# Kernel tuning notes

Measured on AMD Instinct MI355X. Metric: run time of the kernel, lower is better.

Reference implementation:

```python
import jax, jax.numpy as jnp
import numpy as np

N_EXPERTS = 8
D_MODEL = 1024
D_FF = 2048
NUM_TOKENS = 16384


def setup_inputs() -> dict:
    key = jax.random.key(0)
    k1, k2, k3, k4 = jax.random.split(key, 4)
    x = jax.random.normal(k1, (NUM_TOKENS, D_MODEL), dtype=jnp.float32)
    expert_indices = jax.random.randint(k2, (NUM_TOKENS,), 0, N_EXPERTS, dtype=jnp.int32)
    # init per nn.init.normal_(std=0.02)
    gate_up_weight = 0.02 * jax.random.normal(k3, (N_EXPERTS, 2 * D_FF, D_MODEL), dtype=jnp.float32)
    down_weight = 0.02 * jax.random.normal(k4, (N_EXPERTS, D_MODEL, D_FF), dtype=jnp.float32)
    return {"x": x, "expert_indices": expert_indices,
            "gate_up_weight": gate_up_weight, "down_weight": down_weight}


def reference(x, expert_indices, gate_up_weight, down_weight):
    # Faithful math: each token t uses expert e = expert_indices[t]:
    #   combined = x @ gate_up_weight[e].T ; gate, up = split ; h = silu(gate)*up
    #   out = h @ down_weight[e].T
    # Implemented as a fixed loop over the (small) expert set with masked
    # accumulation, avoiding the original's per-token [2F,D] weight gather.
    n_experts = gate_up_weight.shape[0]
    d_ff = down_weight.shape[2]
    out = jnp.zeros((x.shape[0], down_weight.shape[1]), dtype=x.dtype)
    for e in range(n_experts):
        combined = x @ gate_up_weight[e].T                  # [T, 2*d_ff]
        gate, up = combined[:, :d_ff], combined[:, d_ff:]
        hidden = jax.nn.silu(gate) * up                     # [T, d_ff]
        o = hidden @ down_weight[e].T                       # [T, d_model]
        out = out + jnp.where((expert_indices == e)[:, None], o, 0.0)
    return out
```

## Files before the change

### kernel.cpp

```cpp
#include <hip/hip_runtime.h>

#define NTOK 16384
#define DM 1024
#define DFF 2048
#define NE 8

typedef unsigned short u16;
typedef __attribute__((ext_vector_type(8))) short bf16x8;
typedef __attribute__((ext_vector_type(4))) float f32x4;

__device__ __forceinline__ u16 f2bf(float f) {
  unsigned u = __float_as_uint(f);
  u += 0x7fff + ((u >> 16) & 1);
  return (u16)(u >> 16);
}

__device__ __forceinline__ void async16(const void* g, void* l) {
  __builtin_amdgcn_global_load_lds(
      (const __attribute__((address_space(1))) unsigned int*)g,
      (__attribute__((address_space(3))) unsigned int*)l, 16, 0, 0);
}

__global__ void k_count(const int* __restrict__ idx, int* __restrict__ counts) {
  int t = blockIdx.x * 256 + threadIdx.x;
  atomicAdd(&counts[idx[t]], 1);
}

__global__ void k_offsets(int* __restrict__ c) {
  if (threadIdx.x == 0) {
    int acc = 0;
    for (int e = 0; e < NE; e++) { c[8 + e] = acc; c[16 + e] = acc; acc += c[e]; }
  }
}

__global__ void k_scatter(const int* __restrict__ idx, int* __restrict__ cursor,
                          int* __restrict__ tl) {
  int t = blockIdx.x * 256 + threadIdx.x;
  int pos = atomicAdd(&cursor[idx[t]], 1);
  tl[pos] = t;
}

__global__ void k_cvt_all(const float* __restrict__ x, const float* __restrict__ wgu,
                          const float* __restrict__ wd, u16* __restrict__ xb,
                          u16* __restrict__ wgub, u16* __restrict__ wdb) {
  const size_t N1 = (size_t)NTOK * DM;
  const size_t N2 = (size_t)NE * 2 * DFF * DM;
  const size_t N3 = (size_t)NE * DM * DFF;
  const size_t total4 = (N1 + N2 + N3) / 4;
  for (size_t q = (size_t)blockIdx.x * 256 + threadIdx.x; q < total4;
       q += (size_t)gridDim.x * 256) {
    size_t i = q * 4;
    const float* s;
    u16* d;
    if (i < N1) { s = x + i; d = xb + i; }
    else if (i < N1 + N2) { s = wgu + (i - N1); d = wgub + (i - N1); }
    else { s = wd + (i - N1 - N2); d = wdb + (i - N1 - N2); }
    float4 v = *(const float4*)s;
    ushort4 o;
    o.x = f2bf(v.x); o.y = f2bf(v.y); o.z = f2bf(v.z); o.w = f2bf(v.w);
    *(ushort4*)d = o;
  }
}

__global__ __launch_bounds__(512, 2) void k_gemm1(
    const u16* __restrict__ xb, const u16* __restrict__ wgu,
    u16* __restrict__ hid, const int* __restrict__ tl,
    const int* __restrict__ offs, const int* __restrict__ counts) {
  int wg = blockIdx.x;
  int e = wg & 7;
  int r = wg >> 3;
  int bx = r >> 4;
  int by = r & 15;
  int Me = counts[e];
  int m0 = bx * 256;
  if (m0 >= Me) return;
  int n0 = by * 128;
  int oe = offs[e];
  const int* tle = tl + oe;

  int tid = threadIdx.x;
  int lane = tid & 63;
  int wid = tid >> 6;
  int wm = wid >> 2;
  int wn = wid & 3;

  __shared__ u16 lds[2][2][256 * 64];

  int lr = lane >> 3;
  int swz = ((lane & 7) ^ lr) * 8;
  const u16* pA[4];
  const u16* pB[4];
#pragma unroll
  for (int j = 0; j < 4; j++) {
    int c = j * 8 + wid;
    int a = m0 + c * 8 + lr;
    if (a >= Me) a = Me - 1;
    pA[j] = xb + (size_t)tle[a] * DM + swz;
    int b = c * 8 + lr;
    int grow = ((b >> 5) & 1) * DFF + n0 + ((b >> 6) & 3) * 32 + (b & 31);
    pB[j] = wgu + ((size_t)e * 2 * DFF + grow) * DM + swz;
  }

  f32x4 acc[8][4];
#pragma unroll
  for (int m = 0; m < 8; m++)
#pragma unroll
    for (int f = 0; f < 4; f++) acc[m][f] = (f32x4){0.f, 0.f, 0.f, 0.f};

  const int r15 = lane & 15;
  const int hi4 = lane >> 4;
  const int rx = r15 & 7;

#pragma unroll
  for (int j = 0; j < 4; j++) {
    int off = (j * 8 + wid) * 1024;
    async16(pA[j], (char*)&lds[0][0][0] + off);
    async16(pB[j], (char*)&lds[0][1][0] + off);
  }
  asm volatile("s_waitcnt vmcnt(0)" ::: "memory");
  __builtin_amdgcn_s_barrier();
  __builtin_amdgcn_sched_barrier(0);

  int cur = 0;
#pragma unroll 1
  for (int t = 0; t < DM / 64; t++) {
    const char* Ab = (const char*)&lds[cur][0][0];
    const char* Bb = (const char*)&lds[cur][1][0];
    char* LA = (char*)&lds[cur ^ 1][0][0];
    char* LB = (char*)&lds[cur ^ 1][1][0];
    int k1 = (t + 1) * 64;
    bool pf = (t < DM / 64 - 1);
    bf16x8 bfr[4][2];
#pragma unroll
    for (int p = 0; p < 4; p++) {
      if (p == 0) {
#pragma unroll
        for (int f = 0; f < 4; f++)
#pragma unroll
          for (int kk = 0; kk < 2; kk++) {
            int row = wn * 64 + f * 16 + r15;
            bfr[f][kk] = *(const bf16x8*)(Bb + row * 128 + (((kk * 4 + hi4) ^ rx) * 16));
          }
      }
      bf16x8 af[2][2];
#pragma unroll
      for (int i = 0; i < 2; i++)
#pragma unroll
        for (int kk = 0; kk < 2; kk++) {
          int row = wm * 128 + (2 * p + i) * 16 + r15;
          af[i][kk] = *(const bf16x8*)(Ab + row * 128 + (((kk * 4 + hi4) ^ rx) * 16));
        }
      if (pf) {
        int off = (p * 8 + wid) * 1024;
        async16(pA[p] + k1, LA + off);
        async16(pB[p] + k1, LB + off);
      }
      __builtin_amdgcn_s_barrier();
      __builtin_amdgcn_sched_barrier(0);
      __builtin_amdgcn_s_setprio(1);
#pragma unroll
      for (int kk = 0; kk < 2; kk++)
#pragma unroll
        for (int i = 0; i < 2; i++)
#pragma unroll
          for (int f = 0; f < 4; f++)
            acc[2 * p + i][f] = __builtin_amdgcn_mfma_f32_16x16x32_bf16(
                af[i][kk], bfr[f][kk], acc[2 * p + i][f], 0, 0, 0);
      __builtin_amdgcn_s_setprio(0);
      __builtin_amdgcn_sched_barrier(0);
    }
    asm volatile("s_waitcnt vmcnt(0)" ::: "memory");
    __builtin_amdgcn_s_barrier();
    __builtin_amdgcn_sched_barrier(0);
    cur ^= 1;
  }

  int colb = n0 + wn * 32 + r15;
#pragma unroll
  for (int m = 0; m < 8; m++) {
#pragma unroll
    for (int rr = 0; rr < 4; rr++) {
      int gm = m0 + wm * 128 + m * 16 + hi4 * 4 + rr;
      if (gm < Me) {
        size_t rowp = (size_t)(oe + gm) * DFF;
#pragma unroll
        for (int f = 0; f < 2; f++) {
          float g = acc[m][f][rr];
          float u = acc[m][f + 2][rr];
          float s = g / (1.0f + __expf(-g));
          hid[rowp + colb + f * 16] = f2bf(s * u);
        }
      }
    }
  }
}

__global__ __launch_bounds__(512, 2) void k_gemm2(
    const u16* __restrict__ hid, const u16* __restrict__ wd,
    float* __restrict__ out, const int* __restrict__ tl,
    const int* __restrict__ offs, const int* __restrict__ counts) {
  int wg = blockIdx.x;
  int e = wg & 7;
  int r = wg >> 3;
  int bx = r >> 2;
  int by = r & 3;
  int Me = counts[e];
  int m0 = bx * 256;
  if (m0 >= Me) return;
  int n0 = by * 256;
  int oe = offs[e];
  const int* tle = tl + oe;

  int tid = threadIdx.x;
  int lane = tid & 63;
  int wid = tid >> 6;
  int wm = wid >> 2;
  int wn = wid & 3;

  __shared__ u16 lds[2][2][256 * 64];

  int lr = lane >> 3;
  int swz = ((lane & 7) ^ lr) * 8;
  const u16* pA[4];
  const u16* pB[4];
#pragma unroll
  for (int j = 0; j < 4; j++) {
    int c = j * 8 + wid;
    int a = m0 + c * 8 + lr;
    if (a >= Me) a = Me - 1;
    pA[j] = hid + (size_t)(oe + a) * DFF + swz;
    pB[j] = wd + ((size_t)e * DM + n0 + c * 8 + lr) * DFF + swz;
  }

  f32x4 acc[8][4];
#pragma unroll
  for (int m = 0; m < 8; m++)
#pragma unroll
    for (int f = 0; f < 4; f++) acc[m][f] = (f32x4){0.f, 0.f, 0.f, 0.f};

  const int r15 = lane & 15;
  const int hi4 = lane >> 4;
  const int rx = r15 & 7;

#pragma unroll
  for (int j = 0; j < 4; j++) {
    int off = (j * 8 + wid) * 1024;
    async16(pA[j], (char*)&lds[0][0][0] + off);
    async16(pB[j], (char*)&lds[0][1][0] + off);
  }
  asm volatile("s_waitcnt vmcnt(0)" ::: "memory");
  __builtin_amdgcn_s_barrier();
  __builtin_amdgcn_sched_barrier(0);

  int cur = 0;
#pragma unroll 1
  for (int t = 0; t < DFF / 64; t++) {
    const char* Ab = (const char*)&lds[cur][0][0];
    const char* Bb = (const char*)&lds[cur][1][0];
    char* LA = (char*)&lds[cur ^ 1][0][0];
    char* LB = (char*)&lds[cur ^ 1][1][0];
    int k1 = (t + 1) * 64;
    bool pf = (t < DFF / 64 - 1);
    bf16x8 bfr[4][2];
#pragma unroll
    for (int p = 0; p < 4; p++) {
      if (p == 0) {
#pragma unroll
        for (int f = 0; f < 4; f++)
#pragma unroll
          for (int kk = 0; kk < 2; kk++) {
            int row = wn * 64 + f * 16 + r15;
            bfr[f][kk] = *(const bf16x8*)(Bb + row * 128 + (((kk * 4 + hi4) ^ rx) * 16));
          }
      }
      bf16x8 af[2][2];
#pragma unroll
      for (int i = 0; i < 2; i++)
#pragma unroll
        for (int kk = 0; kk < 2; kk++) {
          int row = wm * 128 + (2 * p + i) * 16 + r15;
          af[i][kk] = *(const bf16x8*)(Ab + row * 128 + (((kk * 4 + hi4) ^ rx) * 16));
        }
      if (pf) {
        int off = (p * 8 + wid) * 1024;
        async16(pA[p] + k1, LA + off);
        async16(pB[p] + k1, LB + off);
      }
      __builtin_amdgcn_s_barrier();
      __builtin_amdgcn_sched_barrier(0);
      __builtin_amdgcn_s_setprio(1);
#pragma unroll
      for (int kk = 0; kk < 2; kk++)
#pragma unroll
        for (int i = 0; i < 2; i++)
#pragma unroll
          for (int f = 0; f < 4; f++)
            acc[2 * p + i][f] = __builtin_amdgcn_mfma_f32_16x16x32_bf16(
                af[i][kk], bfr[f][kk], acc[2 * p + i][f], 0, 0, 0);
      __builtin_amdgcn_s_setprio(0);
      __builtin_amdgcn_sched_barrier(0);
    }
    asm volatile("s_waitcnt vmcnt(0)" ::: "memory");
    __builtin_amdgcn_s_barrier();
    __builtin_amdgcn_sched_barrier(0);
    cur ^= 1;
  }

  int colb = n0 + wn * 64 + r15;
#pragma unroll
  for (int m = 0; m < 8; m++) {
#pragma unroll
    for (int rr = 0; rr < 4; rr++) {
      int gm = m0 + wm * 128 + m * 16 + hi4 * 4 + rr;
      if (gm < Me) {
        int tk = tle[gm];
#pragma unroll
        for (int f = 0; f < 4; f++)
          out[(size_t)tk * DM + colb + f * 16] = acc[m][f][rr];
      }
    }
  }
}

extern "C" void kernel_launch(void* const* d_in, const int* in_sizes, int n_in,
                              void* d_out, int out_size, void* d_ws, size_t ws_size,
                              hipStream_t stream) {
  const float* x   = (const float*)d_in[0];
  const int* eidx  = (const int*)d_in[1];
  const float* wgu = (const float*)d_in[2];
  const float* wd  = (const float*)d_in[3];
  float* out = (float*)d_out;
  char* ws = (char*)d_ws;

  int* ctrl = (int*)ws;
  int* toklist = (int*)(ws + 256);
  u16* xb   = (u16*)(ws + 65792);
  u16* wgub = (u16*)(ws + 65792 + 33554432ull);
  u16* wdb  = (u16*)(ws + 65792 + 33554432ull + 67108864ull);
  u16* hid  = (u16*)(ws + 65792 + 33554432ull + 67108864ull + 33554432ull);

  hipMemsetAsync(ws, 0, 256, stream);
  k_count<<<NTOK / 256, 256, 0, stream>>>(eidx, ctrl);
  k_offsets<<<1, 64, 0, stream>>>(ctrl);
  k_scatter<<<NTOK / 256, 256, 0, stream>>>(eidx, ctrl + 16, toklist);

  k_cvt_all<<<2048, 256, 0, stream>>>(x, wgu, wd, xb, wgub, wdb);

  k_gemm1<<<9 * 16 * NE, 512, 0, stream>>>(xb, wgub, hid, toklist, ctrl + 8, ctrl);
  k_gemm2<<<9 * 4 * NE, 512, 0, stream>>>(hid, wdb, out, toklist, ctrl + 8, ctrl);
}
```

Baseline: 499.7 us.

## Fuse fp32-to-bf16 conversion into GEMM tile loads and drop the conversion pass

Removes the standalone kernel that converted x and both weight tensors to bf16. The GEMMs now load fp32 tiles into registers, convert them to bf16, and write them into swizzled LDS, staggered across the four sub-steps of each k-iteration. The block index mapping is also reordered so the M-blocks that share a weight tile run next to each other, which should improve cache reuse of the fp32 weights. The trade-offs are twice the global bytes per tile, many extra registers for staging under a 2-blocks-per-CU launch bound (a spill risk), and rounding that now goes half-up instead of to nearest-even.

```diff
diff --git a/kernel.cpp b/kernel.cpp
--- a/kernel.cpp
+++ b/kernel.cpp
@@ -13,6 +13,21 @@
   unsigned u = __float_as_uint(f);
   u += 0x7fff + ((u >> 16) & 1);
   return (u16)(u >> 16);
+}
+
+__device__ __forceinline__ unsigned pack2(float a, float b) {
+  unsigned ua = __float_as_uint(a) + 0x8000u;
+  unsigned ub = __float_as_uint(b) + 0x8000u;
+  return (ua >> 16) | (ub & 0xffff0000u);
+}
+
+__device__ __forceinline__ bf16x8 cvt8(const float4& a, const float4& b) {
+  union { unsigned u[4]; bf16x8 v; } r;
+  r.u[0] = pack2(a.x, a.y);
+  r.u[1] = pack2(a.z, a.w);
+  r.u[2] = pack2(b.x, b.y);
+  r.u[3] = pack2(b.z, b.w);
+  return r.v;
 }
 
 __device__ __forceinline__ void async16(const void* g, void* l) {
@@ -40,37 +55,15 @@
   tl[pos] = t;
 }
 
-__global__ void k_cvt_all(const float* __restrict__ x, const float* __restrict__ wgu,
-                          const float* __restrict__ wd, u16* __restrict__ xb,
-                          u16* __restrict__ wgub, u16* __restrict__ wdb) {
-  const size_t N1 = (size_t)NTOK * DM;
-  const size_t N2 = (size_t)NE * 2 * DFF * DM;
-  const size_t N3 = (size_t)NE * DM * DFF;
-  const size_t total4 = (N1 + N2 + N3) / 4;
-  for (size_t q = (size_t)blockIdx.x * 256 + threadIdx.x; q < total4;
-       q += (size_t)gridDim.x * 256) {
-    size_t i = q * 4;
-    const float* s;
-    u16* d;
-    if (i < N1) { s = x + i; d = xb + i; }
-    else if (i < N1 + N2) { s = wgu + (i - N1); d = wgub + (i - N1); }
-    else { s = wd + (i - N1 - N2); d = wdb + (i - N1 - N2); }
-    float4 v = *(const float4*)s;
-    ushort4 o;
-    o.x = f2bf(v.x); o.y = f2bf(v.y); o.z = f2bf(v.z); o.w = f2bf(v.w);
-    *(ushort4*)d = o;
-  }
-}
-
 __global__ __launch_bounds__(512, 2) void k_gemm1(
-    const u16* __restrict__ xb, const u16* __restrict__ wgu,
+    const float* __restrict__ x, const float* __restrict__ wgu,
     u16* __restrict__ hid, const int* __restrict__ tl,
     const int* __restrict__ offs, const int* __restrict__ counts) {
   int wg = blockIdx.x;
   int e = wg & 7;
   int r = wg >> 3;
-  int bx = r >> 4;
-  int by = r & 15;
+  int bx = r % 9;
+  int by = r / 9;
   int Me = counts[e];
   int m0 = bx * 256;
   if (m0 >= Me) return;
@@ -87,19 +80,20 @@
   __shared__ u16 lds[2][2][256 * 64];
 
   int lr = lane >> 3;
-  int swz = ((lane & 7) ^ lr) * 8;
-  const u16* pA[4];
-  const u16* pB[4];
+  int l7 = lane & 7;
+  const float* pAx[4];
+  const float* pBx[4];
 #pragma unroll
   for (int j = 0; j < 4; j++) {
     int c = j * 8 + wid;
     int a = m0 + c * 8 + lr;
     if (a >= Me) a = Me - 1;
-    pA[j] = xb + (size_t)tle[a] * DM + swz;
+    pAx[j] = x + (size_t)tle[a] * DM + l7 * 8;
     int b = c * 8 + lr;
     int grow = ((b >> 5) & 1) * DFF + n0 + ((b >> 6) & 3) * 32 + (b & 31);
-    pB[j] = wgu + ((size_t)e * 2 * DFF + grow) * DM + swz;
-  }
+    pBx[j] = wgu + ((size_t)e * 2 * DFF + grow) * DM + l7 * 8;
+  }
+  int stoff = wid * 1024 + lr * 128 + ((l7 ^ lr) * 16);
 
   f32x4 acc[8][4];
 #pragma unroll
@@ -111,15 +105,26 @@
   const int hi4 = lane >> 4;
   const int rx = r15 & 7;
 
-#pragma unroll
-  for (int j = 0; j < 4; j++) {
-    int off = (j * 8 + wid) * 1024;
-    async16(pA[j], (char*)&lds[0][0][0] + off);
-    async16(pB[j], (char*)&lds[0][1][0] + off);
-  }
-  asm volatile("s_waitcnt vmcnt(0)" ::: "memory");
-  __builtin_amdgcn_s_barrier();
-  __builtin_amdgcn_sched_barrier(0);
+  {
+    char* LA = (char*)&lds[0][0][0];
+    char* LB = (char*)&lds[0][1][0];
+    float4 sA[8], sB[8];
+#pragma unroll
+    for (int j = 0; j < 4; j++) {
+      sA[2 * j] = *(const float4*)(pAx[j]);
+      sA[2 * j + 1] = *(const float4*)(pAx[j] + 4);
+      sB[2 * j] = *(const float4*)(pBx[j]);
+      sB[2 * j + 1] = *(const float4*)(pBx[j] + 4);
+    }
+#pragma unroll
+    for (int j = 0; j < 4; j++) {
+      *(bf16x8*)(LA + j * 8192 + stoff) = cvt8(sA[2 * j], sA[2 * j + 1]);
+      *(bf16x8*)(LB + j * 8192 + stoff) = cvt8(sB[2 * j], sB[2 * j + 1]);
+    }
+    asm volatile("s_waitcnt lgkmcnt(0)" ::: "memory");
+    __builtin_amdgcn_s_barrier();
+    __builtin_amdgcn_sched_barrier(0);
+  }
 
   int cur = 0;
 #pragma unroll 1
@@ -130,6 +135,7 @@
     char* LB = (char*)&lds[cur ^ 1][1][0];
     int k1 = (t + 1) * 64;
     bool pf = (t < DM / 64 - 1);
+    float4 sA[8], sB[8];
     bf16x8 bfr[4][2];
 #pragma unroll
     for (int p = 0; p < 4; p++) {
@@ -151,9 +157,27 @@
           af[i][kk] = *(const bf16x8*)(Ab + row * 128 + (((kk * 4 + hi4) ^ rx) * 16));
         }
       if (pf) {
-        int off = (p * 8 + wid) * 1024;
-        async16(pA[p] + k1, LA + off);
-        async16(pB[p] + k1, LB + off);
+        if (p == 0) {
+#pragma unroll
+          for (int j = 0; j < 4; j++) {
+            sA[2 * j] = *(const float4*)(pAx[j] + k1);
+            sA[2 * j + 1] = *(const float4*)(pAx[j] + k1 + 4);
+          }
+        } else if (p == 1) {
+#pragma unroll
+          for (int j = 0; j < 4; j++) {
+            sB[2 * j] = *(const float4*)(pBx[j] + k1);
+            sB[2 * j + 1] = *(const float4*)(pBx[j] + k1 + 4);
+          }
+        } else if (p == 2) {
+#pragma unroll
+          for (int j = 0; j < 4; j++)
+            *(bf16x8*)(LA + j * 8192 + stoff) = cvt8(sA[2 * j], sA[2 * j + 1]);
+        } else {
+#pragma unroll
+          for (int j = 0; j < 4; j++)
+            *(bf16x8*)(LB + j * 8192 + stoff) = cvt8(sB[2 * j], sB[2 * j + 1]);
+        }
       }
       __builtin_amdgcn_s_barrier();
       __builtin_amdgcn_sched_barrier(0);
@@ -169,7 +193,7 @@
       __builtin_amdgcn_s_setprio(0);
       __builtin_amdgcn_sched_barrier(0);
     }
-    asm volatile("s_waitcnt vmcnt(0)" ::: "memory");
+    asm volatile("s_waitcnt lgkmcnt(0)" ::: "memory");
     __builtin_amdgcn_s_barrier();
     __builtin_amdgcn_sched_barrier(0);
     cur ^= 1;
@@ -196,14 +220,14 @@
 }
 
 __global__ __launch_bounds__(512, 2) void k_gemm2(
-    const u16* __restrict__ hid, const u16* __restrict__ wd,
+    const u16* __restrict__ hid, const float* __restrict__ wd,
     float* __restrict__ out, const int* __restrict__ tl,
     const int* __restrict__ offs, const int* __restrict__ counts) {
   int wg = blockIdx.x;
   int e = wg & 7;
   int r = wg >> 3;
-  int bx = r >> 2;
-  int by = r & 3;
+  int bx = r % 9;
+  int by = r / 9;
   int Me = counts[e];
   int m0 = bx * 256;
   if (m0 >= Me) return;
@@ -220,17 +244,19 @@
   __shared__ u16 lds[2][2][256 * 64];
 
   int lr = lane >> 3;
-  int swz = ((lane & 7) ^ lr) * 8;
+  int l7 = lane & 7;
+  int swz = (l7 ^ lr) * 8;
   const u16* pA[4];
-  const u16* pB[4];
+  const float* pBx[4];
 #pragma unroll
   for (int j = 0; j < 4; j++) {
     int c = j * 8 + wid;
     int a = m0 + c * 8 + lr;
     if (a >= Me) a = Me - 1;
     pA[j] = hid + (size_t)(oe + a) * DFF + swz;
-    pB[j] = wd + ((size_t)e * DM + n0 + c * 8 + lr) * DFF + swz;
-  }
+    pBx[j] = wd + ((size_t)e * DM + n0 + c * 8 + lr) * DFF + l7 * 8;
+  }
+  int stoff = wid * 1024 + lr * 128 + ((l7 ^ lr) * 16);
 
   f32x4 acc[8][4];
 #pragma unroll
@@ -242,15 +268,25 @@
   const int hi4 = lane >> 4;
   const int rx = r15 & 7;
 
-#pragma unroll
-  for (int j = 0; j < 4; j++) {
-    int off = (j * 8 + wid) * 1024;
-    async16(pA[j], (char*)&lds[0][0][0] + off);
-    async16(pB[j], (char*)&lds[0][1][0] + off);
-  }
-  asm volatile("s_waitcnt vmcnt(0)" ::: "memory");
-  __builtin_amdgcn_s_barrier();
-  __builtin_amdgcn_sched_barrier(0);
+  {
+    char* LA = (char*)&lds[0][0][0];
+    char* LB = (char*)&lds[0][1][0];
+#pragma unroll
+    for (int j = 0; j < 4; j++)
+      async16(pA[j], LA + (j * 8 + wid) * 1024);
+    float4 sB[8];
+#pragma unroll
+    for (int j = 0; j < 4; j++) {
+      sB[2 * j] = *(const float4*)(pBx[j]);
+      sB[2 * j + 1] = *(const float4*)(pBx[j] + 4);
+    }
+#pragma unroll
+    for (int j = 0; j < 4; j++)
+      *(bf16x8*)(LB + j * 8192 + stoff) = cvt8(sB[2 * j], sB[2 * j + 1]);
+    asm volatile("s_waitcnt vmcnt(0) lgkmcnt(0)" ::: "memory");
+    __builtin_amdgcn_s_barrier();
+    __builtin_amdgcn_sched_barrier(0);
+  }
 
   int cur = 0;
 #pragma unroll 1
@@ -261,6 +297,7 @@
     char* LB = (char*)&lds[cur ^ 1][1][0];
     int k1 = (t + 1) * 64;
     bool pf = (t < DFF / 64 - 1);
+    float4 sB[8];
     bf16x8 bfr[4][2];
 #pragma unroll
     for (int p = 0; p < 4; p++) {
@@ -282,9 +319,29 @@
           af[i][kk] = *(const bf16x8*)(Ab + row * 128 + (((kk * 4 + hi4) ^ rx) * 16));
         }
       if (pf) {
-        int off = (p * 8 + wid) * 1024;
-        async16(pA[p] + k1, LA + off);
-        async16(pB[p] + k1, LB + off);
+        if (p == 0) {
+#pragma unroll
+          for (int j = 0; j < 2; j++) {
+            async16(pA[j] + k1, LA + (j * 8 + wid) * 1024);
+            sB[2 * j] = *(const float4*)(pBx[j] + k1);
+            sB[2 * j + 1] = *(const float4*)(pBx[j] + k1 + 4);
+          }
+        } else if (p == 1) {
+#pragma unroll
+          for (int j = 2; j < 4; j++) {
+            async16(pA[j] + k1, LA + (j * 8 + wid) * 1024);
+            sB[2 * j] = *(const float4*)(pBx[j] + k1);
+            sB[2 * j + 1] = *(const float4*)(pBx[j] + k1 + 4);
+          }
+        } else if (p == 2) {
+#pragma unroll
+          for (int j = 0; j < 2; j++)
+            *(bf16x8*)(LB + j * 8192 + stoff) = cvt8(sB[2 * j], sB[2 * j + 1]);
+        } else {
+#pragma unroll
+          for (int j = 2; j < 4; j++)
+            *(bf16x8*)(LB + j * 8192 + stoff) = cvt8(sB[2 * j], sB[2 * j + 1]);
+        }
       }
       __builtin_amdgcn_s_barrier();
       __builtin_amdgcn_sched_barrier(0);
@@ -300,7 +357,7 @@
       __builtin_amdgcn_s_setprio(0);
       __builtin_amdgcn_sched_barrier(0);
     }
-    asm volatile("s_waitcnt vmcnt(0)" ::: "memory");
+    asm volatile("s_waitcnt vmcnt(0) lgkmcnt(0)" ::: "memory");
     __builtin_amdgcn_s_barrier();
     __builtin_amdgcn_sched_barrier(0);
     cur ^= 1;
@@ -334,18 +391,13 @@
 
   int* ctrl = (int*)ws;
   int* toklist = (int*)(ws + 256);
-  u16* xb   = (u16*)(ws + 65792);
-  u16* wgub = (u16*)(ws + 65792 + 33554432ull);
-  u16* wdb  = (u16*)(ws + 65792 + 33554432ull + 67108864ull);
-  u16* hid  = (u16*)(ws + 65792 + 33554432ull + 67108864ull + 33554432ull);
+  u16* hid = (u16*)(ws + 65792);
 
   hipMemsetAsync(ws, 0, 256, stream);
   k_count<<<NTOK / 256, 256, 0, stream>>>(eidx, ctrl);
   k_offsets<<<1, 64, 0, stream>>>(ctrl);
   k_scatter<<<NTOK / 256, 256, 0, stream>>>(eidx, ctrl + 16, toklist);
 
-  k_cvt_all<<<2048, 256, 0, stream>>>(x, wgu, wd, xb, wgub, wdb);
-
-  k_gemm1<<<9 * 16 * NE, 512, 0, stream>>>(xb, wgub, hid, toklist, ctrl + 8, ctrl);
-  k_gemm2<<<9 * 4 * NE, 512, 0, stream>>>(hid, wdb, out, toklist, ctrl + 8, ctrl);
-}
+  k_gemm1<<<9 * 16 * NE, 512, 0, stream>>>(x, wgu, hid, toklist, ctrl + 8, ctrl);
+  k_gemm2<<<9 * 4 * NE, 512, 0, stream>>>(hid, wd, out, toklist, ctrl + 8, ctrl);
+}
```

Result: slower. 1.778 ms (+255.9%).
